# Kernel optimization log

Measured on AMD Instinct MI355X. Metric: run time of the kernel, lower is better.

The kernel has to match this reference:

```python
import jax, jax.numpy as jnp
import numpy as np
from jax import lax

VOCAB = 100000
INPUT_DIM = 100
HIDDEN_DIM = 10
OUTPUT_DIM = 1
BATCH = 1024
SEQ = 512


def setup_inputs() -> dict:
    key = jax.random.key(0)
    ks = jax.random.split(key, 8)
    bound_ih = 1.0 / np.sqrt(HIDDEN_DIM)
    inp = {
        "x": jax.random.randint(ks[0], (BATCH, SEQ), 0, VOCAB, dtype=jnp.int32),
        "emb": jax.random.normal(ks[1], (VOCAB, INPUT_DIM), dtype=jnp.float32),
        "W_ih": jax.random.uniform(ks[2], (HIDDEN_DIM, INPUT_DIM), jnp.float32, -bound_ih, bound_ih),
        "b_ih": jax.random.uniform(ks[3], (HIDDEN_DIM,), jnp.float32, -bound_ih, bound_ih),
        "W_hh": jax.random.uniform(ks[4], (HIDDEN_DIM, HIDDEN_DIM), jnp.float32, -bound_ih, bound_ih),
        "b_hh": jax.random.uniform(ks[5], (HIDDEN_DIM,), jnp.float32, -bound_ih, bound_ih),
        "W_fc": jax.random.uniform(ks[6], (OUTPUT_DIM, HIDDEN_DIM), jnp.float32, -bound_ih, bound_ih),
        "b_fc": jax.random.uniform(ks[7], (OUTPUT_DIM,), jnp.float32, -bound_ih, bound_ih),
    }
    return inp


def reference(x, emb, W_ih, b_ih, W_hh, b_hh, W_fc, b_fc):
    # Embedding lookup: [B, S, INPUT_DIM]
    xe = emb[x]
    # Precompute input projection for all timesteps in one GEMM: [B, S, H]
    pre = jnp.einsum("bsd,hd->bsh", xe, W_ih) + b_ih

    def step(h, p_t):
        # h: [B, H], p_t: [B, H]
        h_new = jax.nn.relu(p_t + h @ W_hh.T + b_hh)
        return h_new, None

    h0 = jnp.zeros((x.shape[0], W_hh.shape[0]), dtype=pre.dtype)
    hn, _ = lax.scan(step, h0, jnp.swapaxes(pre, 0, 1))  # scan over time
    # torch returns hn of shape [layer_dim=1, B, H]; fc + sigmoid on hn
    out = jax.nn.sigmoid(hn @ W_fc.T + b_fc)[None, :, :]  # [1, B, 1]
    return out
```

## Files before the change

### kernel.cpp

```cpp
#include <hip/hip_runtime.h>
#include <hip/hip_bf16.h>
#include <math.h>

#define VOCAB 100000
#define INPUT_DIM 100
#define HIDDEN_DIM 10
#define BATCH 1024
#define SEQ 512

#define ROWS_PER_BLK 64
#define LDS_PITCH 102

__global__ __launch_bounds__(256) void proj_kernel(
    const float* __restrict__ emb, const float* __restrict__ W_ih,
    const float* __restrict__ b_ih, const float* __restrict__ b_hh,
    float* __restrict__ proj) {
  __shared__ float se[ROWS_PER_BLK * LDS_PITCH];

  const int t = threadIdx.x;
  const size_t base = (size_t)blockIdx.x * (ROWS_PER_BLK * INPUT_DIM);
  const size_t TOT = (size_t)VOCAB * INPUT_DIM;

#pragma unroll
  for (int l = 0; l < 7; ++l) {
    int n4 = t + 256 * l;
    if (n4 < 1600) {
      int n = n4 * 4;
      size_t g = base + n;
      float4 val;
      if (g + 3 < TOT) {
        val = *(const float4*)(emb + g);
      } else {
        val.x = (g + 0 < TOT) ? emb[g + 0] : 0.f;
        val.y = (g + 1 < TOT) ? emb[g + 1] : 0.f;
        val.z = (g + 2 < TOT) ? emb[g + 2] : 0.f;
        val.w = (g + 3 < TOT) ? emb[g + 3] : 0.f;
      }
      int r0 = n / 100, k0 = n - r0 * 100;
      se[r0 * LDS_PITCH + k0] = val.x;
      int n1 = n + 1; int r1 = n1 / 100, k1 = n1 - r1 * 100;
      se[r1 * LDS_PITCH + k1] = val.y;
      int n2 = n + 2; int r2 = n2 / 100, k2 = n2 - r2 * 100;
      se[r2 * LDS_PITCH + k2] = val.z;
      int n3 = n + 3; int r3 = n3 / 100, k3 = n3 - r3 * 100;
      se[r3 * LDS_PITCH + k3] = val.w;
    }
  }
  __syncthreads();

  const int row = t & 63;
  const int q = __builtin_amdgcn_readfirstlane(threadIdx.x >> 6);
  const int v = blockIdx.x * ROWS_PER_BLK + row;
  const int iq2 = (q < 2) ? (q + 8) : q;

  const float* W0 = W_ih + q * INPUT_DIM;
  const float* W1 = W_ih + (q + 4) * INPUT_DIM;
  const float* W2 = W_ih + iq2 * INPUT_DIM;

  float acc0 = b_ih[q] + b_hh[q];
  float acc1 = b_ih[q + 4] + b_hh[q + 4];
  float acc2 = b_ih[iq2] + b_hh[iq2];

  const float* er = se + row * LDS_PITCH;
#pragma unroll
  for (int k = 0; k < INPUT_DIM; ++k) {
    float e = er[k];
    acc0 = fmaf(e, W0[k], acc0);
    acc1 = fmaf(e, W1[k], acc1);
    acc2 = fmaf(e, W2[k], acc2);
  }

  if (v < VOCAB) {
    float* pv = proj + (size_t)v * HIDDEN_DIM;
    pv[q] = acc0;
    pv[q + 4] = acc1;
    if (q < 2) pv[q + 8] = acc2;
  }
}

__global__ __launch_bounds__(256, 1) void scan_kernel(
    const int* __restrict__ x, const float* __restrict__ proj,
    const float* __restrict__ W_hh, const float* __restrict__ W_fc,
    const float* __restrict__ b_fc, float* __restrict__ out) {
  __shared__ int sIdx[4][SEQ];

  int lane = threadIdx.x & 63;
  int widx = threadIdx.x >> 6;
  int b = __builtin_amdgcn_readfirstlane((int)(blockIdx.x * 4 + widx));
  int i = (lane < HIDDEN_DIM) ? lane : 0;

  float Wr[HIDDEN_DIM];
#pragma unroll
  for (int j = 0; j < HIDDEN_DIM; ++j) Wr[j] = W_hh[i * HIDDEN_DIM + j];
  float wfc = (lane < HIDDEN_DIM) ? W_fc[lane] : 0.f;

  const int4* xb4 = (const int4*)(x + (size_t)b * SEQ);
  int4* s4 = (int4*)(sIdx[widx]);
  s4[lane] = xb4[lane];
  s4[64 + lane] = xb4[64 + lane];

  const float* projLane = proj + i;
  float h = 0.f;

#define LOADIDX(Q0, Q1, base)                              \
  {                                                        \
    int bc_ = (base) <= (SEQ - 8) ? (base) : (SEQ - 8);    \
    Q0 = s4[bc_ >> 2];                                     \
    Q1 = s4[(bc_ >> 2) + 1];                               \
  }
#define GATHER(P, Q0, Q1)                                  \
  P[0] = projLane[(unsigned)Q0.x * 10u];                   \
  P[1] = projLane[(unsigned)Q0.y * 10u];                   \
  P[2] = projLane[(unsigned)Q0.z * 10u];                   \
  P[3] = projLane[(unsigned)Q0.w * 10u];                   \
  P[4] = projLane[(unsigned)Q1.x * 10u];                   \
  P[5] = projLane[(unsigned)Q1.y * 10u];                   \
  P[6] = projLane[(unsigned)Q1.z * 10u];                   \
  P[7] = projLane[(unsigned)Q1.w * 10u];
#define COMPUTE(P)                                         \
  _Pragma("unroll") for (int u = 0; u < 8; ++u) {          \
    float hj[HIDDEN_DIM];                                  \
    _Pragma("unroll") for (int j = 0; j < HIDDEN_DIM; ++j) \
      hj[j] = __uint_as_float(                             \
          __builtin_amdgcn_readlane(__float_as_uint(h), j)); \
    float a0 = fmaf(Wr[0], hj[0], P[u]);                   \
    float a1 = Wr[1] * hj[1];                              \
    a0 = fmaf(Wr[2], hj[2], a0);                           \
    a1 = fmaf(Wr[3], hj[3], a1);                           \
    a0 = fmaf(Wr[4], hj[4], a0);                           \
    a1 = fmaf(Wr[5], hj[5], a1);                           \
    a0 = fmaf(Wr[6], hj[6], a0);                           \
    a1 = fmaf(Wr[7], hj[7], a1);                           \
    a0 = fmaf(Wr[8], hj[8], a0);                           \
    a1 = fmaf(Wr[9], hj[9], a1);                           \
    h = fmaxf(a0 + a1, 0.f);                               \
  }

  int4 Ia0, Ia1, Ib0, Ib1, Ic0, Ic1, Id0, Id1;
  float pA[8], pB[8], pC[8], pD[8];

  LOADIDX(Ia0, Ia1, 0) LOADIDX(Ib0, Ib1, 8) LOADIDX(Ic0, Ic1, 16)
  GATHER(pA, Ia0, Ia1) GATHER(pB, Ib0, Ib1) GATHER(pC, Ic0, Ic1)
  LOADIDX(Id0, Id1, 24)

  for (int tt = 0; tt < SEQ; tt += 32) {
    GATHER(pD, Id0, Id1) LOADIDX(Ia0, Ia1, tt + 32) COMPUTE(pA)
    GATHER(pA, Ia0, Ia1) LOADIDX(Ib0, Ib1, tt + 40) COMPUTE(pB)
    GATHER(pB, Ib0, Ib1) LOADIDX(Ic0, Ic1, tt + 48) COMPUTE(pC)
    GATHER(pC, Ic0, Ic1) LOADIDX(Id0, Id1, tt + 56) COMPUTE(pD)
  }
#undef LOADIDX
#undef GATHER
#undef COMPUTE

  float prod = wfc * h;
  float z = 0.f;
#pragma unroll
  for (int j = 0; j < HIDDEN_DIM; ++j)
    z += __uint_as_float(__builtin_amdgcn_readlane(__float_as_uint(prod), j));
  if (lane == 0) out[b] = 1.f / (1.f + expf(-(z + b_fc[0])));
}

extern "C" void kernel_launch(void* const* d_in, const int* in_sizes, int n_in,
                              void* d_out, int out_size, void* d_ws, size_t ws_size,
                              hipStream_t stream) {
  const int*   x    = (const int*)d_in[0];
  const float* emb  = (const float*)d_in[1];
  const float* W_ih = (const float*)d_in[2];
  const float* b_ih = (const float*)d_in[3];
  const float* W_hh = (const float*)d_in[4];
  const float* b_hh = (const float*)d_in[5];
  const float* W_fc = (const float*)d_in[6];
  const float* b_fc = (const float*)d_in[7];
  float* out = (float*)d_out;

  float* proj = (float*)d_ws;

  int blocksA = (VOCAB + ROWS_PER_BLK - 1) / ROWS_PER_BLK;
  proj_kernel<<<blocksA, 256, 0, stream>>>(emb, W_ih, b_ih, b_hh, proj);
  proj_kernel<<<blocksA, 256, 0, stream>>>(emb, W_ih, b_ih, b_hh, proj);

  int blocksB = BATCH / 4;
  scan_kernel<<<blocksB, 256, 0, stream>>>(x, proj, W_hh, W_fc, b_fc, out);
}
```

Baseline: 139.6 us.

## Split scan into producer/consumer waves with LDS ring; drop duplicate proj launch

Restructures the recurrent scan so one wave gathers projected rows for the next 32-step chunk into a double-buffered LDS ring while the other wave runs the serial recurrence from LDS. Each block now handles one batch row with 128 threads. A redundant second launch of the projection kernel is removed. The ring adds per-chunk barriers and LDS reads on the critical path, in exchange for coalesced float2 gathers overlapped with compute.

```diff
diff --git a/kernel.cpp b/kernel.cpp
--- a/kernel.cpp
+++ b/kernel.cpp
@@ -78,87 +78,94 @@
   }
 }
 
-__global__ __launch_bounds__(256, 1) void scan_kernel(
+#define CHUNK 32
+#define NCHUNK (SEQ / CHUNK)
+#define RPITCH 12
+
+__global__ __launch_bounds__(128, 1) void scan_kernel(
     const int* __restrict__ x, const float* __restrict__ proj,
     const float* __restrict__ W_hh, const float* __restrict__ W_fc,
     const float* __restrict__ b_fc, float* __restrict__ out) {
-  __shared__ int sIdx[4][SEQ];
+  __shared__ int sIdx[SEQ];
+  __shared__ float ring[2][CHUNK * RPITCH];
 
-  int lane = threadIdx.x & 63;
-  int widx = threadIdx.x >> 6;
-  int b = __builtin_amdgcn_readfirstlane((int)(blockIdx.x * 4 + widx));
-  int i = (lane < HIDDEN_DIM) ? lane : 0;
+  const int t = threadIdx.x;
+  const int lane = t & 63;
+  const int widx = t >> 6;
+  const int b = blockIdx.x;
+
+  ((int4*)sIdx)[t] = ((const int4*)(x + (size_t)b * SEQ))[t];
+  __syncthreads();
+
+  const int i = (lane < HIDDEN_DIM) ? lane : 0;
 
   float Wr[HIDDEN_DIM];
+  float wfc = 0.f;
+  if (widx == 0) {
 #pragma unroll
-  for (int j = 0; j < HIDDEN_DIM; ++j) Wr[j] = W_hh[i * HIDDEN_DIM + j];
-  float wfc = (lane < HIDDEN_DIM) ? W_fc[lane] : 0.f;
-
-  const int4* xb4 = (const int4*)(x + (size_t)b * SEQ);
-  int4* s4 = (int4*)(sIdx[widx]);
-  s4[lane] = xb4[lane];
-  s4[64 + lane] = xb4[64 + lane];
-
-  const float* projLane = proj + i;
-  float h = 0.f;
-
-#define LOADIDX(Q0, Q1, base)                              \
-  {                                                        \
-    int bc_ = (base) <= (SEQ - 8) ? (base) : (SEQ - 8);    \
-    Q0 = s4[bc_ >> 2];                                     \
-    Q1 = s4[(bc_ >> 2) + 1];                               \
-  }
-#define GATHER(P, Q0, Q1)                                  \
-  P[0] = projLane[(unsigned)Q0.x * 10u];                   \
-  P[1] = projLane[(unsigned)Q0.y * 10u];                   \
-  P[2] = projLane[(unsigned)Q0.z * 10u];                   \
-  P[3] = projLane[(unsigned)Q0.w * 10u];                   \
-  P[4] = projLane[(unsigned)Q1.x * 10u];                   \
-  P[5] = projLane[(unsigned)Q1.y * 10u];                   \
-  P[6] = projLane[(unsigned)Q1.z * 10u];                   \
-  P[7] = projLane[(unsigned)Q1.w * 10u];
-#define COMPUTE(P)                                         \
-  _Pragma("unroll") for (int u = 0; u < 8; ++u) {          \
-    float hj[HIDDEN_DIM];                                  \
-    _Pragma("unroll") for (int j = 0; j < HIDDEN_DIM; ++j) \
-      hj[j] = __uint_as_float(                             \
-          __builtin_amdgcn_readlane(__float_as_uint(h), j)); \
-    float a0 = fmaf(Wr[0], hj[0], P[u]);                   \
-    float a1 = Wr[1] * hj[1];                              \
-    a0 = fmaf(Wr[2], hj[2], a0);                           \
-    a1 = fmaf(Wr[3], hj[3], a1);                           \
-    a0 = fmaf(Wr[4], hj[4], a0);                           \
-    a1 = fmaf(Wr[5], hj[5], a1);                           \
-    a0 = fmaf(Wr[6], hj[6], a0);                           \
-    a1 = fmaf(Wr[7], hj[7], a1);                           \
-    a0 = fmaf(Wr[8], hj[8], a0);                           \
-    a1 = fmaf(Wr[9], hj[9], a1);                           \
-    h = fmaxf(a0 + a1, 0.f);                               \
+    for (int j = 0; j < HIDDEN_DIM; ++j) Wr[j] = W_hh[i * HIDDEN_DIM + j];
+    wfc = (lane < HIDDEN_DIM) ? W_fc[lane] : 0.f;
   }
 
-  int4 Ia0, Ia1, Ib0, Ib1, Ic0, Ic1, Id0, Id1;
-  float pA[8], pB[8], pC[8], pD[8];
+#define FILL(src)                                                   \
+  {                                                                 \
+    const int rbase_ = (src) * CHUNK;                               \
+    float* dst_ = ring[(src) & 1];                                  \
+    _Pragma("unroll") for (int pass = 0; pass < 3; ++pass) {        \
+      int j_ = pass * 64 + lane;                                    \
+      if (j_ < CHUNK * 5) {                                         \
+        int r_ = j_ / 5;                                            \
+        int p_ = j_ - r_ * 5;                                       \
+        int idx_ = sIdx[rbase_ + r_];                               \
+        float2 val_ =                                               \
+            *(const float2*)(proj + (size_t)idx_ * 10u + p_ * 2);   \
+        *(float2*)(dst_ + r_ * RPITCH + p_ * 2) = val_;             \
+      }                                                             \
+    }                                                               \
+  }
 
-  LOADIDX(Ia0, Ia1, 0) LOADIDX(Ib0, Ib1, 8) LOADIDX(Ic0, Ic1, 16)
-  GATHER(pA, Ia0, Ia1) GATHER(pB, Ib0, Ib1) GATHER(pC, Ic0, Ic1)
-  LOADIDX(Id0, Id1, 24)
+  if (widx == 1) FILL(0);
+  __syncthreads();
 
-  for (int tt = 0; tt < SEQ; tt += 32) {
-    GATHER(pD, Id0, Id1) LOADIDX(Ia0, Ia1, tt + 32) COMPUTE(pA)
-    GATHER(pA, Ia0, Ia1) LOADIDX(Ib0, Ib1, tt + 40) COMPUTE(pB)
-    GATHER(pB, Ib0, Ib1) LOADIDX(Ic0, Ic1, tt + 48) COMPUTE(pC)
-    GATHER(pC, Ic0, Ic1) LOADIDX(Id0, Id1, tt + 56) COMPUTE(pD)
+  float h = 0.f;
+  for (int c = 0; c < NCHUNK; ++c) {
+    if (widx == 1) {
+      if (c + 1 < NCHUNK) FILL(c + 1);
+    } else {
+      const float* rg = ring[c & 1] + i;
+#pragma unroll
+      for (int tt = 0; tt < CHUNK; ++tt) {
+        float pt = rg[tt * RPITCH];
+        float hj[HIDDEN_DIM];
+#pragma unroll
+        for (int j = 0; j < HIDDEN_DIM; ++j)
+          hj[j] = __uint_as_float(
+              __builtin_amdgcn_readlane(__float_as_uint(h), j));
+        float a0 = fmaf(Wr[0], hj[0], pt);
+        float a1 = Wr[1] * hj[1];
+        a0 = fmaf(Wr[2], hj[2], a0);
+        a1 = fmaf(Wr[3], hj[3], a1);
+        a0 = fmaf(Wr[4], hj[4], a0);
+        a1 = fmaf(Wr[5], hj[5], a1);
+        a0 = fmaf(Wr[6], hj[6], a0);
+        a1 = fmaf(Wr[7], hj[7], a1);
+        a0 = fmaf(Wr[8], hj[8], a0);
+        a1 = fmaf(Wr[9], hj[9], a1);
+        h = fmaxf(a0 + a1, 0.f);
+      }
+    }
+    __syncthreads();
   }
-#undef LOADIDX
-#undef GATHER
-#undef COMPUTE
+#undef FILL
 
-  float prod = wfc * h;
-  float z = 0.f;
+  if (widx == 0) {
+    float prod = wfc * h;
+    float z = 0.f;
 #pragma unroll
-  for (int j = 0; j < HIDDEN_DIM; ++j)
-    z += __uint_as_float(__builtin_amdgcn_readlane(__float_as_uint(prod), j));
-  if (lane == 0) out[b] = 1.f / (1.f + expf(-(z + b_fc[0])));
+    for (int j = 0; j < HIDDEN_DIM; ++j)
+      z += __uint_as_float(__builtin_amdgcn_readlane(__float_as_uint(prod), j));
+    if (lane == 0) out[b] = 1.f / (1.f + expf(-(z + b_fc[0])));
+  }
 }
 
 extern "C" void kernel_launch(void* const* d_in, const int* in_sizes, int n_in,
@@ -178,8 +185,6 @@
 
   int blocksA = (VOCAB + ROWS_PER_BLK - 1) / ROWS_PER_BLK;
   proj_kernel<<<blocksA, 256, 0, stream>>>(emb, W_ih, b_ih, b_hh, proj);
-  proj_kernel<<<blocksA, 256, 0, stream>>>(emb, W_ih, b_ih, b_hh, proj);
 
-  int blocksB = BATCH / 4;
-  scan_kernel<<<blocksB, 256, 0, stream>>>(x, proj, W_hh, W_fc, b_fc, out);
+  scan_kernel<<<BATCH, 128, 0, stream>>>(x, proj, W_hh, W_fc, b_fc, out);
 }
```

Result: no change. 138.0 us (-1.1%).
